# Performance work log

Measured on AMD Instinct MI355X. Metric: run time of the kernel, lower is better.

The kernel has to match this reference:

```python
import jax, jax.numpy as jnp
import numpy as np

B, T, D = 32, 2048, 1024


def setup_inputs() -> dict:
    key = jax.random.key(0)
    k1, k2, k3, k4, k5, k6 = jax.random.split(key, 6)
    return {
        "keys": jax.random.normal(k1, (B, T, D), dtype=jnp.float32),
        "value": jax.random.normal(k2, (B, T, D), dtype=jnp.float32),
        "query": jax.random.normal(k3, (B, D), dtype=jnp.float32),
        "weight_feedback": jax.random.normal(k4, (B, T, D), dtype=jnp.float32),
        "v": jax.random.normal(k5, (D,), dtype=jnp.float32) / np.sqrt(D),
        "enc_seq_len": jax.random.randint(k6, (B,), 1, T + 1, dtype=jnp.int32),
    }


def reference(keys, value, query, weight_feedback, v, enc_seq_len):
    # energies = v^T tanh(key + query + weight_feedback)  -> [B, T]
    hidden = jnp.tanh(keys + query[:, None, :] + weight_feedback)  # [B,T,D]
    energies = jnp.einsum("btd,d->bt", hidden, v)                  # [B,T]
    # length mask + softmax over time
    mask = jnp.arange(energies.shape[1])[None, :] < enc_seq_len[:, None]  # [B,T]
    energies = jnp.where(mask, energies, -jnp.inf)
    weights = jax.nn.softmax(energies, axis=1)                      # [B,T]
    # context = weights^T value -> [B, D_v]
    context = jnp.einsum("bt,btd->bd", weights, value)
    return context, weights[:, :, None]
```

## Files before the change

### kernel.cpp

```cpp
#include <hip/hip_runtime.h>
#include <math.h>

#define BB 32
#define TT 2048
#define DD 1024

#define EROWS_PER_WAVE  8
#define EROWS_PER_BLOCK 32
#define CCHUNK 64
#define NCHUNK (TT / CCHUNK)

__device__ __forceinline__ float fast_tanh(float x) {
    float e = __expf(2.0f * x);
    return 1.0f - __fdividef(2.0f, e + 1.0f);
}

__global__ __launch_bounds__(256) void energies_kernel(
    const float* __restrict__ keys, const float* __restrict__ query,
    const float* __restrict__ wf, const float* __restrict__ v,
    const int* __restrict__ lenp, float* __restrict__ eout)
{
    const int b = blockIdx.y;
    const int L = lenp[b];
    const int t0 = blockIdx.x * EROWS_PER_BLOCK;
    if (t0 >= L) return;

    const int lane = threadIdx.x & 63;
    const int wv   = threadIdx.x >> 6;
    const int d0   = lane * 4;

    float4 q[4], vv[4];
    #pragma unroll
    for (int j = 0; j < 4; j++) {
        q[j]  = *(const float4*)(query + (size_t)b * DD + j * 256 + d0);
        vv[j] = *(const float4*)(v + j * 256 + d0);
    }

    const int tBeg = t0 + wv * EROWS_PER_WAVE;
    const int tEnd = min(tBeg + EROWS_PER_WAVE, L);
    for (int t = tBeg; t < tEnd; t++) {
        const size_t row = ((size_t)b * TT + t) * DD;
        float4 k[4], w[4];
        #pragma unroll
        for (int j = 0; j < 4; j++) {
            k[j] = *(const float4*)(keys + row + j * 256 + d0);
            w[j] = *(const float4*)(wf   + row + j * 256 + d0);
        }
        float s = 0.0f;
        #pragma unroll
        for (int j = 0; j < 4; j++) {
            s += vv[j].x * fast_tanh(k[j].x + q[j].x + w[j].x);
            s += vv[j].y * fast_tanh(k[j].y + q[j].y + w[j].y);
            s += vv[j].z * fast_tanh(k[j].z + q[j].z + w[j].z);
            s += vv[j].w * fast_tanh(k[j].w + q[j].w + w[j].w);
        }
        #pragma unroll
        for (int off = 32; off > 0; off >>= 1)
            s += __shfl_xor(s, off, 64);
        if (lane == 0) eout[(size_t)b * TT + t] = s;
    }
}

__global__ __launch_bounds__(256) void softmax_kernel(
    const int* __restrict__ lenp, float* __restrict__ wrow_all)
{
    const int b = blockIdx.x;
    const int L = lenp[b];
    float* wrow = wrow_all + (size_t)b * TT;

    float e[8];
    float m = -INFINITY;
    #pragma unroll
    for (int i = 0; i < 8; i++) {
        const int t = threadIdx.x + i * 256;
        e[i] = (t < L) ? wrow[t] : -INFINITY;
        m = fmaxf(m, e[i]);
    }
    #pragma unroll
    for (int off = 1; off < 64; off <<= 1) m = fmaxf(m, __shfl_xor(m, off, 64));
    __shared__ float redm[4];
    const int wv = threadIdx.x >> 6;
    if ((threadIdx.x & 63) == 0) redm[wv] = m;
    __syncthreads();
    m = fmaxf(fmaxf(redm[0], redm[1]), fmaxf(redm[2], redm[3]));

    float s = 0.0f;
    #pragma unroll
    for (int i = 0; i < 8; i++) {
        e[i] = (e[i] == -INFINITY) ? 0.0f : __expf(e[i] - m);
        s += e[i];
    }
    #pragma unroll
    for (int off = 1; off < 64; off <<= 1) s += __shfl_xor(s, off, 64);
    __shared__ float reds[4];
    if ((threadIdx.x & 63) == 0) reds[wv] = s;
    __syncthreads();
    s = reds[0] + reds[1] + reds[2] + reds[3];
    const float inv = 1.0f / s;

    #pragma unroll
    for (int i = 0; i < 8; i++)
        wrow[threadIdx.x + i * 256] = e[i] * inv;
}

__global__ __launch_bounds__(256) void context_partial_kernel(
    const float* __restrict__ value, const float* __restrict__ weights,
    const int* __restrict__ lenp, float* __restrict__ partial)
{
    const int b = blockIdx.y;
    const int L = lenp[b];
    const int c = blockIdx.x;
    const int t0 = c * CCHUNK;
    if (t0 >= L) return;
    const int tend = min(t0 + CCHUNK, L);
    const int d = threadIdx.x * 4;

    __shared__ float wsh[CCHUNK];
    if (threadIdx.x < CCHUNK) {
        const int t = t0 + threadIdx.x;
        wsh[threadIdx.x] = (t < L) ? weights[(size_t)b * TT + t] : 0.0f;
    }
    __syncthreads();

    float4 acc = make_float4(0.f, 0.f, 0.f, 0.f);
    #pragma unroll 4
    for (int t = t0; t < tend; t++) {
        const float wt = wsh[t - t0];
        const float4 v4 = *(const float4*)(value + ((size_t)b * TT + t) * DD + d);
        acc.x += wt * v4.x; acc.y += wt * v4.y;
        acc.z += wt * v4.z; acc.w += wt * v4.w;
    }
    *(float4*)(partial + ((size_t)c * BB + b) * DD + d) = acc;
}

__global__ __launch_bounds__(256) void context_reduce_kernel(
    const float* __restrict__ partial, const int* __restrict__ lenp,
    float* __restrict__ context)
{
    const int b = blockIdx.x;
    const int nch = (lenp[b] + CCHUNK - 1) / CCHUNK;
    const int d = threadIdx.x * 4;
    float4 acc = make_float4(0.f, 0.f, 0.f, 0.f);
    for (int c = 0; c < nch; c++) {
        const float4 p = *(const float4*)(partial + ((size_t)c * BB + b) * DD + d);
        acc.x += p.x; acc.y += p.y; acc.z += p.z; acc.w += p.w;
    }
    *(float4*)(context + (size_t)b * DD + d) = acc;
}

__global__ __launch_bounds__(256) void context_atomic_kernel(
    const float* __restrict__ value, const float* __restrict__ weights,
    const int* __restrict__ lenp, float* __restrict__ context)
{
    const int b = blockIdx.y;
    const int L = lenp[b];
    const int t0 = blockIdx.x * CCHUNK;
    if (t0 >= L) return;
    const int tend = min(t0 + CCHUNK, L);
    const int d = threadIdx.x * 4;

    float4 acc = make_float4(0.f, 0.f, 0.f, 0.f);
    for (int t = t0; t < tend; t++) {
        const float w = weights[(size_t)b * TT + t];
        const float4 v4 = *(const float4*)(value + ((size_t)b * TT + t) * DD + d);
        acc.x += w * v4.x; acc.y += w * v4.y;
        acc.z += w * v4.z; acc.w += w * v4.w;
    }
    float* dst = context + (size_t)b * DD + d;
    atomicAdd(dst + 0, acc.x);
    atomicAdd(dst + 1, acc.y);
    atomicAdd(dst + 2, acc.z);
    atomicAdd(dst + 3, acc.w);
}

extern "C" void kernel_launch(void* const* d_in, const int* in_sizes, int n_in,
                              void* d_out, int out_size, void* d_ws, size_t ws_size,
                              hipStream_t stream) {
    const float* keys  = (const float*)d_in[0];
    const float* value = (const float*)d_in[1];
    const float* query = (const float*)d_in[2];
    const float* wf    = (const float*)d_in[3];
    const float* v     = (const float*)d_in[4];
    const int*   lenp  = (const int*)d_in[5];

    float* out      = (float*)d_out;
    float* context  = out;
    float* weights  = out + BB * DD;

    energies_kernel<<<dim3(TT / EROWS_PER_BLOCK, BB), 256, 0, stream>>>(
        keys, query, wf, v, lenp, weights);
    softmax_kernel<<<BB, 256, 0, stream>>>(lenp, weights);

    const size_t need = (size_t)NCHUNK * BB * DD * sizeof(float);
    if (d_ws != nullptr && ws_size >= need) {
        float* partial = (float*)d_ws;
        context_partial_kernel<<<dim3(NCHUNK, BB), 256, 0, stream>>>(
            value, weights, lenp, partial);
        context_reduce_kernel<<<BB, 256, 0, stream>>>(partial, lenp, context);
    } else {
        hipMemsetAsync(context, 0, (size_t)BB * DD * sizeof(float), stream);
        context_atomic_kernel<<<dim3(NCHUNK, BB), 256, 0, stream>>>(
            value, weights, lenp, context);
    }
}
```

Measured before the change: 613.6 us.

## Process two energy rows per wave and use atomic context accumulation

The energies kernel now handles two time rows per loop iteration, issuing more independent loads before the tanh/dot work and writing both results with one float2 store. The context stage drops the workspace partial buffer and separate reduce kernel. It accumulates per-chunk partials directly into the output with atomicAdd after a memset, using the shared-memory weight staging. This removes the partial write/read traffic and one launch, in exchange for float atomics and order-dependent summation.

```diff
diff --git a/kernel.cpp b/kernel.cpp
--- a/kernel.cpp
+++ b/kernel.cpp
@@ -8,7 +8,6 @@
 #define EROWS_PER_WAVE  8
 #define EROWS_PER_BLOCK 32
 #define CCHUNK 64
-#define NCHUNK (TT / CCHUNK)
 
 __device__ __forceinline__ float fast_tanh(float x) {
     float e = __expf(2.0f * x);
@@ -38,26 +37,58 @@
 
     const int tBeg = t0 + wv * EROWS_PER_WAVE;
     const int tEnd = min(tBeg + EROWS_PER_WAVE, L);
-    for (int t = tBeg; t < tEnd; t++) {
-        const size_t row = ((size_t)b * TT + t) * DD;
-        float4 k[4], w[4];
+
+    int t = tBeg;
+    for (; t + 2 <= tEnd; t += 2) {
+        const size_t r0 = ((size_t)b * TT + t) * DD;
+        const size_t r1 = r0 + DD;
+        float4 k0[4], w0[4], k1[4], w1[4];
         #pragma unroll
         for (int j = 0; j < 4; j++) {
-            k[j] = *(const float4*)(keys + row + j * 256 + d0);
-            w[j] = *(const float4*)(wf   + row + j * 256 + d0);
+            k0[j] = *(const float4*)(keys + r0 + j * 256 + d0);
+            w0[j] = *(const float4*)(wf   + r0 + j * 256 + d0);
+            k1[j] = *(const float4*)(keys + r1 + j * 256 + d0);
+            w1[j] = *(const float4*)(wf   + r1 + j * 256 + d0);
         }
-        float s = 0.0f;
+        float s0 = 0.0f, s1 = 0.0f;
         #pragma unroll
         for (int j = 0; j < 4; j++) {
-            s += vv[j].x * fast_tanh(k[j].x + q[j].x + w[j].x);
-            s += vv[j].y * fast_tanh(k[j].y + q[j].y + w[j].y);
-            s += vv[j].z * fast_tanh(k[j].z + q[j].z + w[j].z);
-            s += vv[j].w * fast_tanh(k[j].w + q[j].w + w[j].w);
+            s0 += vv[j].x * fast_tanh(k0[j].x + q[j].x + w0[j].x);
+            s0 += vv[j].y * fast_tanh(k0[j].y + q[j].y + w0[j].y);
+            s0 += vv[j].z * fast_tanh(k0[j].z + q[j].z + w0[j].z);
+            s0 += vv[j].w * fast_tanh(k0[j].w + q[j].w + w0[j].w);
+            s1 += vv[j].x * fast_tanh(k1[j].x + q[j].x + w1[j].x);
+            s1 += vv[j].y * fast_tanh(k1[j].y + q[j].y + w1[j].y);
+            s1 += vv[j].z * fast_tanh(k1[j].z + q[j].z + w1[j].z);
+            s1 += vv[j].w * fast_tanh(k1[j].w + q[j].w + w1[j].w);
         }
         #pragma unroll
-        for (int off = 32; off > 0; off >>= 1)
-            s += __shfl_xor(s, off, 64);
-        if (lane == 0) eout[(size_t)b * TT + t] = s;
+        for (int off = 32; off > 0; off >>= 1) {
+            s0 += __shfl_xor(s0, off, 64);
+            s1 += __shfl_xor(s1, off, 64);
+        }
+        if (lane == 0)
+            *(float2*)(eout + (size_t)b * TT + t) = make_float2(s0, s1);
+    }
+    if (t < tEnd) {
+        const size_t r0 = ((size_t)b * TT + t) * DD;
+        float4 k0[4], w0[4];
+        #pragma unroll
+        for (int j = 0; j < 4; j++) {
+            k0[j] = *(const float4*)(keys + r0 + j * 256 + d0);
+            w0[j] = *(const float4*)(wf   + r0 + j * 256 + d0);
+        }
+        float s0 = 0.0f;
+        #pragma unroll
+        for (int j = 0; j < 4; j++) {
+            s0 += vv[j].x * fast_tanh(k0[j].x + q[j].x + w0[j].x);
+            s0 += vv[j].y * fast_tanh(k0[j].y + q[j].y + w0[j].y);
+            s0 += vv[j].z * fast_tanh(k0[j].z + q[j].z + w0[j].z);
+            s0 += vv[j].w * fast_tanh(k0[j].w + q[j].w + w0[j].w);
+        }
+        #pragma unroll
+        for (int off = 32; off > 0; off >>= 1) s0 += __shfl_xor(s0, off, 64);
+        if (lane == 0) eout[(size_t)b * TT + t] = s0;
     }
 }
 
@@ -103,14 +134,13 @@
         wrow[threadIdx.x + i * 256] = e[i] * inv;
 }
 
-__global__ __launch_bounds__(256) void context_partial_kernel(
+__global__ __launch_bounds__(256) void context_kernel(
     const float* __restrict__ value, const float* __restrict__ weights,
-    const int* __restrict__ lenp, float* __restrict__ partial)
+    const int* __restrict__ lenp, float* __restrict__ context)
 {
     const int b = blockIdx.y;
     const int L = lenp[b];
-    const int c = blockIdx.x;
-    const int t0 = c * CCHUNK;
+    const int t0 = blockIdx.x * CCHUNK;
     if (t0 >= L) return;
     const int tend = min(t0 + CCHUNK, L);
     const int d = threadIdx.x * 4;
@@ -129,42 +159,6 @@
         const float4 v4 = *(const float4*)(value + ((size_t)b * TT + t) * DD + d);
         acc.x += wt * v4.x; acc.y += wt * v4.y;
         acc.z += wt * v4.z; acc.w += wt * v4.w;
-    }
-    *(float4*)(partial + ((size_t)c * BB + b) * DD + d) = acc;
-}
-
-__global__ __launch_bounds__(256) void context_reduce_kernel(
-    const float* __restrict__ partial, const int* __restrict__ lenp,
-    float* __restrict__ context)
-{
-    const int b = blockIdx.x;
-    const int nch = (lenp[b] + CCHUNK - 1) / CCHUNK;
-    const int d = threadIdx.x * 4;
-    float4 acc = make_float4(0.f, 0.f, 0.f, 0.f);
-    for (int c = 0; c < nch; c++) {
-        const float4 p = *(const float4*)(partial + ((size_t)c * BB + b) * DD + d);
-        acc.x += p.x; acc.y += p.y; acc.z += p.z; acc.w += p.w;
-    }
-    *(float4*)(context + (size_t)b * DD + d) = acc;
-}
-
-__global__ __launch_bounds__(256) void context_atomic_kernel(
-    const float* __restrict__ value, const float* __restrict__ weights,
-    const int* __restrict__ lenp, float* __restrict__ context)
-{
-    const int b = blockIdx.y;
-    const int L = lenp[b];
-    const int t0 = blockIdx.x * CCHUNK;
-    if (t0 >= L) return;
-    const int tend = min(t0 + CCHUNK, L);
-    const int d = threadIdx.x * 4;
-
-    float4 acc = make_float4(0.f, 0.f, 0.f, 0.f);
-    for (int t = t0; t < tend; t++) {
-        const float w = weights[(size_t)b * TT + t];
-        const float4 v4 = *(const float4*)(value + ((size_t)b * TT + t) * DD + d);
-        acc.x += w * v4.x; acc.y += w * v4.y;
-        acc.z += w * v4.z; acc.w += w * v4.w;
     }
     float* dst = context + (size_t)b * DD + d;
     atomicAdd(dst + 0, acc.x);
@@ -187,19 +181,11 @@
     float* context  = out;
     float* weights  = out + BB * DD;
 
+    hipMemsetAsync(context, 0, (size_t)BB * DD * sizeof(float), stream);
+
     energies_kernel<<<dim3(TT / EROWS_PER_BLOCK, BB), 256, 0, stream>>>(
         keys, query, wf, v, lenp, weights);
     softmax_kernel<<<BB, 256, 0, stream>>>(lenp, weights);
-
-    const size_t need = (size_t)NCHUNK * BB * DD * sizeof(float);
-    if (d_ws != nullptr && ws_size >= need) {
-        float* partial = (float*)d_ws;
-        context_partial_kernel<<<dim3(NCHUNK, BB), 256, 0, stream>>>(
-            value, weights, lenp, partial);
-        context_reduce_kernel<<<BB, 256, 0, stream>>>(partial, lenp, context);
-    } else {
-        hipMemsetAsync(context, 0, (size_t)BB * DD * sizeof(float), stream);
-        context_atomic_kernel<<<dim3(NCHUNK, BB), 256, 0, stream>>>(
-            value, weights, lenp, context);
-    }
+    context_kernel<<<dim3(TT / CCHUNK, BB), 256, 0, stream>>>(
+        value, weights, lenp, context);
 }
```

Result: slower. 632.5 us (+3.1%).
